# Kernel tuning notes

Hardware: AMD Instinct MI355X
Metric: run time of the kernel (lower is better)

## Reference

```python
import jax, jax.numpy as jnp
import numpy as np

N = 500_000
EMB = 256
G = 4096


def setup_inputs() -> dict:
    key = jax.random.key(0)
    k1, k2, k3, k4, k5, k6 = jax.random.split(key, 6)
    values = jax.random.normal(k1, (N, EMB), dtype=jnp.float32)
    indices = jnp.sort(jax.random.randint(k2, (N,), 0, G, dtype=jnp.int64))
    # Linear params (torch Linear: y = x @ W.T + b); stored pre-transposed.
    lim_g = 1.0 / np.sqrt(EMB)
    gate_w = jax.random.uniform(k3, (EMB, 1), jnp.float32, -lim_g, lim_g)
    gate_b = jax.random.uniform(k4, (1,), jnp.float32, -lim_g, lim_g)
    attn_w = jax.random.uniform(k5, (EMB, EMB), jnp.float32, -lim_g, lim_g)
    attn_b = jax.random.uniform(k6, (EMB,), jnp.float32, -lim_g, lim_g)
    return {
        "values": values,
        "indices": indices,
        "num_graphs": G,
        "gate_w": gate_w,
        "gate_b": gate_b,
        "attn_w": attn_w,
        "attn_b": attn_b,
    }


def reference(values, indices, num_graphs, gate_w, gate_b, attn_w, attn_b):
    # Gate scores: [N, 1]
    s = values @ gate_w + gate_b
    # Segmented softmax over nodes grouped by graph id (numerically stable).
    seg_max = jax.ops.segment_max(s, indices, num_segments=num_graphs)  # [G, 1]
    e = jnp.exp(s - seg_max[indices])                                   # [N, 1]
    denom = jax.ops.segment_sum(e, indices, num_segments=num_graphs)   # [G, 1]
    w = e / denom[indices]                                              # [N, 1]
    # Attention projection and weighted segment sum.
    a = values @ attn_w + attn_b                                        # [N, EMB]
    out = jax.ops.segment_sum(w * a, indices, num_segments=num_graphs)  # [G, EMB]
    return out
```

## Files before the change

### kernel.cpp

```cpp
#include <hip/hip_runtime.h>
#include <math.h>

#define EMB 256

typedef float f32x4 __attribute__((ext_vector_type(4)));

__global__ void k_bounds(const int* __restrict__ idx, int* __restrict__ seg_start,
                         int n, int g) {
    int t = blockIdx.x * blockDim.x + threadIdx.x;
    if (t > g) return;
    int lo = 0, hi = n;
    while (lo < hi) {
        int mid = (lo + hi) >> 1;
        if (idx[mid] < t) lo = mid + 1; else hi = mid;
    }
    seg_start[t] = lo;
}

__global__ void __launch_bounds__(256) k_fused(const float* __restrict__ vals,
                                               const float* __restrict__ gate_w,
                                               const float* __restrict__ gate_b,
                                               const int* __restrict__ seg_start,
                                               float* __restrict__ wvec) {
    const int g = blockIdx.x;
    const int start = seg_start[g], end = seg_start[g + 1];
    const int cnt = end - start;
    const int t = threadIdx.x;
    const int lane = t & 63, w = t >> 6;

    __shared__ float m_s[4], d_s[4];
    __shared__ float partial[4][EMB];

    if (cnt <= 0) {
        wvec[(size_t)g * EMB + t] = 0.0f;
        return;
    }

    const f32x4 gw = *reinterpret_cast<const f32x4*>(gate_w + lane * 4);
    const float gb = gate_b[0];

    float m = -INFINITY, d = 0.0f;
    f32x4 acc = {0.f, 0.f, 0.f, 0.f};

    for (int j = start + w * 8; j < end; j += 32) {
        f32x4 v[8];
        #pragma unroll
        for (int r = 0; r < 8; ++r) v[r] = (f32x4){0.f, 0.f, 0.f, 0.f};
        const float* p0 = vals + (size_t)j * EMB + lane * 4;
        if (j + 7 < end) {
            #pragma unroll
            for (int r = 0; r < 8; ++r)
                v[r] = __builtin_nontemporal_load(
                    reinterpret_cast<const f32x4*>(p0 + r * EMB));
        } else {
            #pragma unroll
            for (int r = 0; r < 8; ++r)
                if (j + r < end)
                    v[r] = __builtin_nontemporal_load(
                        reinterpret_cast<const f32x4*>(p0 + r * EMB));
        }

        float s[8];
        #pragma unroll
        for (int r = 0; r < 8; ++r)
            s[r] = v[r].x * gw.x + v[r].y * gw.y + v[r].z * gw.z + v[r].w * gw.w;
        #pragma unroll
        for (int o = 1; o < 64; o <<= 1) {
            #pragma unroll
            for (int r = 0; r < 8; ++r) s[r] += __shfl_xor(s[r], o);
        }
        #pragma unroll
        for (int r = 0; r < 8; ++r) s[r] += gb;
        if (j + 7 >= end) {
            #pragma unroll
            for (int r = 1; r < 8; ++r)
                if (j + r >= end) s[r] = -INFINITY;
        }

        float mx = s[0];
        #pragma unroll
        for (int r = 1; r < 8; ++r) mx = fmaxf(mx, s[r]);
        if (mx > m) {
            const float sc = __expf(m - mx);
            d *= sc;
            acc.x *= sc; acc.y *= sc; acc.z *= sc; acc.w *= sc;
            m = mx;
        }
        float e[8];
        #pragma unroll
        for (int r = 0; r < 8; ++r) e[r] = __expf(s[r] - m);
        #pragma unroll
        for (int r = 0; r < 8; ++r) d += e[r];
        #pragma unroll
        for (int r = 0; r < 8; ++r) {
            acc.x += e[r] * v[r].x;
            acc.y += e[r] * v[r].y;
            acc.z += e[r] * v[r].z;
            acc.w += e[r] * v[r].w;
        }
    }

    if (lane == 0) m_s[w] = m;
    __syncthreads();
    const float M = fmaxf(fmaxf(m_s[0], m_s[1]), fmaxf(m_s[2], m_s[3]));
    const float f = __expf(m - M);
    if (lane == 0) d_s[w] = d * f;
    acc.x *= f; acc.y *= f; acc.z *= f; acc.w *= f;
    *reinterpret_cast<f32x4*>(&partial[w][lane * 4]) = acc;
    __syncthreads();
    const float dt = d_s[0] + d_s[1] + d_s[2] + d_s[3];
    wvec[(size_t)g * EMB + t] =
        (partial[0][t] + partial[1][t] + partial[2][t] + partial[3][t]) / dt;
}

__global__ void __launch_bounds__(256) k_gemm(const float* __restrict__ A,
                                              const float* __restrict__ W,
                                              const float* __restrict__ bias,
                                              const int* __restrict__ seg_start,
                                              float* __restrict__ out) {
    __shared__ float A_s[64][68];
    __shared__ float B_s[64][64];
    const int bid = blockIdx.x;
    const int row0 = (bid >> 2) * 64;
    const int col0 = (bid & 3) * 64;
    const int t = threadIdx.x;
    const int ty = t >> 4, tx = t & 15;

    float acc[4][4] = {};

    for (int kc = 0; kc < EMB; kc += 64) {
        #pragma unroll
        for (int l = t; l < 64 * 16; l += 256) {
            int r = l >> 4, c4 = (l & 15) << 2;
            float4 v = *reinterpret_cast<const float4*>(
                A + (size_t)(row0 + r) * EMB + kc + c4);
            *reinterpret_cast<float4*>(&A_s[r][c4]) = v;
        }
        #pragma unroll
        for (int l = t; l < 64 * 16; l += 256) {
            int r = l >> 4, c4 = (l & 15) << 2;
            *reinterpret_cast<float4*>(&B_s[r][c4]) =
                *reinterpret_cast<const float4*>(
                    W + (size_t)(kc + r) * EMB + col0 + c4);
        }
        __syncthreads();

        #pragma unroll
        for (int k = 0; k < 64; k += 4) {
            float a[4][4], b[4][4];
            #pragma unroll
            for (int i = 0; i < 4; ++i)
                *reinterpret_cast<float4*>(a[i]) =
                    *reinterpret_cast<const float4*>(&A_s[ty * 4 + i][k]);
            #pragma unroll
            for (int kk = 0; kk < 4; ++kk)
                *reinterpret_cast<float4*>(b[kk]) =
                    *reinterpret_cast<const float4*>(&B_s[k + kk][tx * 4]);
            #pragma unroll
            for (int i = 0; i < 4; ++i)
                #pragma unroll
                for (int kk = 0; kk < 4; ++kk)
                    #pragma unroll
                    for (int j = 0; j < 4; ++j)
                        acc[i][j] += a[i][kk] * b[kk][j];
        }
        __syncthreads();
    }

    const float4 b4 = *reinterpret_cast<const float4*>(bias + col0 + tx * 4);
    #pragma unroll
    for (int i = 0; i < 4; ++i) {
        const int r = row0 + ty * 4 + i;
        const float bs = (seg_start[r + 1] - seg_start[r]) > 0 ? 1.0f : 0.0f;
        float4 o;
        o.x = acc[i][0] + bs * b4.x;
        o.y = acc[i][1] + bs * b4.y;
        o.z = acc[i][2] + bs * b4.z;
        o.w = acc[i][3] + bs * b4.w;
        *reinterpret_cast<float4*>(out + (size_t)r * EMB + col0 + tx * 4) = o;
    }
}

extern "C" void kernel_launch(void* const* d_in, const int* in_sizes, int n_in,
                              void* d_out, int out_size, void* d_ws, size_t ws_size,
                              hipStream_t stream) {
    const float* vals   = (const float*)d_in[0];
    const int*   idx    = (const int*)d_in[1];
    const float* gate_w = (const float*)d_in[3];
    const float* gate_b = (const float*)d_in[4];
    const float* attn_w = (const float*)d_in[5];
    const float* attn_b = (const float*)d_in[6];
    float* out = (float*)d_out;

    const int n = in_sizes[1];
    const int g = out_size / EMB;

    int*   seg_start = (int*)d_ws;
    float* wvec = (float*)((char*)d_ws + (((g + 1) * 4 + 15) & ~15));

    k_bounds<<<(g + 256) / 256, 256, 0, stream>>>(idx, seg_start, n, g);
    k_fused<<<g, 256, 0, stream>>>(vals, gate_w, gate_b, seg_start, wvec);
    k_gemm<<<(g / 64) * 4, 256, 0, stream>>>(wvec, attn_w, attn_b, seg_start, out);
}
```

Measured before the change: 109.1 us.

## Build segment bounds by boundary scan and use persistent multi-segment blocks

Segment start offsets are now computed with one thread per index, each writing the boundaries between adjacent elements, in place of one binary search per segment. The fused softmax/weighted-sum kernel now runs on a fixed grid of 1024 blocks, each handling a contiguous run of segments in a loop, rather than one block per segment. This cuts block launch overhead and the serial latency of binary search, but it reduces the number of blocks in flight for the bandwidth-bound pass over the values. The boundary scan reads the whole index array.

```diff
diff --git a/kernel.cpp b/kernel.cpp
--- a/kernel.cpp
+++ b/kernel.cpp
@@ -5,112 +5,117 @@
 
 typedef float f32x4 __attribute__((ext_vector_type(4)));
 
-__global__ void k_bounds(const int* __restrict__ idx, int* __restrict__ seg_start,
-                         int n, int g) {
-    int t = blockIdx.x * blockDim.x + threadIdx.x;
-    if (t > g) return;
-    int lo = 0, hi = n;
-    while (lo < hi) {
-        int mid = (lo + hi) >> 1;
-        if (idx[mid] < t) lo = mid + 1; else hi = mid;
-    }
-    seg_start[t] = lo;
+__global__ void k_bounds_scan(const int* __restrict__ idx, int* __restrict__ seg_start,
+                              int n, int g) {
+    int i = blockIdx.x * blockDim.x + threadIdx.x;
+    if (i >= n) return;
+    const int a = idx[i];
+    const int b = (i + 1 < n) ? idx[i + 1] : g;
+    if (i == 0)
+        for (int q = 0; q <= a; ++q) seg_start[q] = 0;
+    for (int q = a + 1; q <= b; ++q) seg_start[q] = i + 1;
 }
 
 __global__ void __launch_bounds__(256) k_fused(const float* __restrict__ vals,
                                                const float* __restrict__ gate_w,
                                                const float* __restrict__ gate_b,
                                                const int* __restrict__ seg_start,
-                                               float* __restrict__ wvec) {
-    const int g = blockIdx.x;
-    const int start = seg_start[g], end = seg_start[g + 1];
-    const int cnt = end - start;
+                                               float* __restrict__ wvec,
+                                               int G) {
     const int t = threadIdx.x;
     const int lane = t & 63, w = t >> 6;
 
     __shared__ float m_s[4], d_s[4];
     __shared__ float partial[4][EMB];
 
-    if (cnt <= 0) {
-        wvec[(size_t)g * EMB + t] = 0.0f;
-        return;
-    }
-
     const f32x4 gw = *reinterpret_cast<const f32x4*>(gate_w + lane * 4);
     const float gb = gate_b[0];
 
-    float m = -INFINITY, d = 0.0f;
-    f32x4 acc = {0.f, 0.f, 0.f, 0.f};
-
-    for (int j = start + w * 8; j < end; j += 32) {
-        f32x4 v[8];
-        #pragma unroll
-        for (int r = 0; r < 8; ++r) v[r] = (f32x4){0.f, 0.f, 0.f, 0.f};
-        const float* p0 = vals + (size_t)j * EMB + lane * 4;
-        if (j + 7 < end) {
-            #pragma unroll
-            for (int r = 0; r < 8; ++r)
-                v[r] = __builtin_nontemporal_load(
-                    reinterpret_cast<const f32x4*>(p0 + r * EMB));
-        } else {
-            #pragma unroll
-            for (int r = 0; r < 8; ++r)
-                if (j + r < end)
+    const int per = (G + gridDim.x - 1) / gridDim.x;
+    const int g0 = blockIdx.x * per;
+    const int g1 = min(g0 + per, G);
+
+    for (int g = g0; g < g1; ++g) {
+        const int start = seg_start[g], end = seg_start[g + 1];
+
+        if (end <= start) {
+            wvec[(size_t)g * EMB + t] = 0.0f;
+            continue;
+        }
+
+        float m = -INFINITY, d = 0.0f;
+        f32x4 acc = {0.f, 0.f, 0.f, 0.f};
+
+        for (int j = start + w * 8; j < end; j += 32) {
+            f32x4 v[8];
+            #pragma unroll
+            for (int r = 0; r < 8; ++r) v[r] = (f32x4){0.f, 0.f, 0.f, 0.f};
+            const float* p0 = vals + (size_t)j * EMB + lane * 4;
+            if (j + 7 < end) {
+                #pragma unroll
+                for (int r = 0; r < 8; ++r)
                     v[r] = __builtin_nontemporal_load(
                         reinterpret_cast<const f32x4*>(p0 + r * EMB));
-        }
-
-        float s[8];
-        #pragma unroll
-        for (int r = 0; r < 8; ++r)
-            s[r] = v[r].x * gw.x + v[r].y * gw.y + v[r].z * gw.z + v[r].w * gw.w;
-        #pragma unroll
-        for (int o = 1; o < 64; o <<= 1) {
-            #pragma unroll
-            for (int r = 0; r < 8; ++r) s[r] += __shfl_xor(s[r], o);
-        }
-        #pragma unroll
-        for (int r = 0; r < 8; ++r) s[r] += gb;
-        if (j + 7 >= end) {
-            #pragma unroll
-            for (int r = 1; r < 8; ++r)
-                if (j + r >= end) s[r] = -INFINITY;
-        }
-
-        float mx = s[0];
-        #pragma unroll
-        for (int r = 1; r < 8; ++r) mx = fmaxf(mx, s[r]);
-        if (mx > m) {
-            const float sc = __expf(m - mx);
-            d *= sc;
-            acc.x *= sc; acc.y *= sc; acc.z *= sc; acc.w *= sc;
-            m = mx;
-        }
-        float e[8];
-        #pragma unroll
-        for (int r = 0; r < 8; ++r) e[r] = __expf(s[r] - m);
-        #pragma unroll
-        for (int r = 0; r < 8; ++r) d += e[r];
-        #pragma unroll
-        for (int r = 0; r < 8; ++r) {
-            acc.x += e[r] * v[r].x;
-            acc.y += e[r] * v[r].y;
-            acc.z += e[r] * v[r].z;
-            acc.w += e[r] * v[r].w;
-        }
+            } else {
+                #pragma unroll
+                for (int r = 0; r < 8; ++r)
+                    if (j + r < end)
+                        v[r] = __builtin_nontemporal_load(
+                            reinterpret_cast<const f32x4*>(p0 + r * EMB));
+            }
+
+            float s[8];
+            #pragma unroll
+            for (int r = 0; r < 8; ++r)
+                s[r] = v[r].x * gw.x + v[r].y * gw.y + v[r].z * gw.z + v[r].w * gw.w;
+            #pragma unroll
+            for (int o = 1; o < 64; o <<= 1) {
+                #pragma unroll
+                for (int r = 0; r < 8; ++r) s[r] += __shfl_xor(s[r], o);
+            }
+            #pragma unroll
+            for (int r = 0; r < 8; ++r) s[r] += gb;
+            if (j + 7 >= end) {
+                #pragma unroll
+                for (int r = 1; r < 8; ++r)
+                    if (j + r >= end) s[r] = -INFINITY;
+            }
+
+            float mx = s[0];
+            #pragma unroll
+            for (int r = 1; r < 8; ++r) mx = fmaxf(mx, s[r]);
+            if (mx > m) {
+                const float sc = __expf(m - mx);
+                d *= sc;
+                acc.x *= sc; acc.y *= sc; acc.z *= sc; acc.w *= sc;
+                m = mx;
+            }
+            float e[8];
+            #pragma unroll
+            for (int r = 0; r < 8; ++r) e[r] = __expf(s[r] - m);
+            #pragma unroll
+            for (int r = 0; r < 8; ++r) d += e[r];
+            #pragma unroll
+            for (int r = 0; r < 8; ++r) {
+                acc.x += e[r] * v[r].x;
+                acc.y += e[r] * v[r].y;
+                acc.z += e[r] * v[r].z;
+                acc.w += e[r] * v[r].w;
+            }
+        }
+
+        if (lane == 0) m_s[w] = m;
+        __syncthreads();
+        const float M = fmaxf(fmaxf(m_s[0], m_s[1]), fmaxf(m_s[2], m_s[3]));
+        const float f = __expf(m - M);
+        if (lane == 0) d_s[w] = d * f;
+        acc.x *= f; acc.y *= f; acc.z *= f; acc.w *= f;
+        *reinterpret_cast<f32x4*>(&partial[w][lane * 4]) = acc;
+        __syncthreads();
+        const float dt = d_s[0] + d_s[1] + d_s[2] + d_s[3];
+        wvec[(size_t)g * EMB + t] =
+            (partial[0][t] + partial[1][t] + partial[2][t] + partial[3][t]) / dt;
     }
-
-    if (lane == 0) m_s[w] = m;
-    __syncthreads();
-    const float M = fmaxf(fmaxf(m_s[0], m_s[1]), fmaxf(m_s[2], m_s[3]));
-    const float f = __expf(m - M);
-    if (lane == 0) d_s[w] = d * f;
-    acc.x *= f; acc.y *= f; acc.z *= f; acc.w *= f;
-    *reinterpret_cast<f32x4*>(&partial[w][lane * 4]) = acc;
-    __syncthreads();
-    const float dt = d_s[0] + d_s[1] + d_s[2] + d_s[3];
-    wvec[(size_t)g * EMB + t] =
-        (partial[0][t] + partial[1][t] + partial[2][t] + partial[3][t]) / dt;
 }
 
 __global__ void __launch_bounds__(256) k_gemm(const float* __restrict__ A,
@@ -198,7 +203,7 @@
     int*   seg_start = (int*)d_ws;
     float* wvec = (float*)((char*)d_ws + (((g + 1) * 4 + 15) & ~15));
 
-    k_bounds<<<(g + 256) / 256, 256, 0, stream>>>(idx, seg_start, n, g);
-    k_fused<<<g, 256, 0, stream>>>(vals, gate_w, gate_b, seg_start, wvec);
+    k_bounds_scan<<<(n + 255) / 256, 256, 0, stream>>>(idx, seg_start, n, g);
+    k_fused<<<1024, 256, 0, stream>>>(vals, gate_w, gate_b, seg_start, wvec, g);
     k_gemm<<<(g / 64) * 4, 256, 0, stream>>>(wvec, attn_w, attn_b, seg_start, out);
 }
```

Result: slower. 125.6 us (+15.2%).
